# Optimization experiments

Measured on AMD Instinct MI355X. Metric: run time of the kernel, lower is better.

Reference implementation:

```python
import jax, jax.numpy as jnp
import numpy as np
import math

B, S, D, H = 2, 2048, 1024, 16
DH = D // H

def setup_inputs() -> dict:
    key = jax.random.key(0)
    ks = jax.random.split(key, 12)
    s = 1.0 / math.sqrt(D)
    return {
        "q": jax.random.normal(ks[0], (B, S, D), jnp.float32),
        "k": jax.random.normal(ks[1], (B, S, D), jnp.float32),
        "v": jax.random.normal(ks[2], (B, S, D), jnp.float32),
        "mask": jnp.tril(jnp.ones((S, S), dtype=bool)),  # causal mask
        "Wq": jax.random.normal(ks[3], (D, D), jnp.float32) * s,
        "bq": jnp.zeros((D,), jnp.float32),
        "Wk": jax.random.normal(ks[4], (D, D), jnp.float32) * s,
        "bk": jnp.zeros((D,), jnp.float32),
        "Wv": jax.random.normal(ks[5], (D, D), jnp.float32) * s,
        "bv": jnp.zeros((D,), jnp.float32),
        "Wo": jax.random.normal(ks[6], (D, D), jnp.float32) * s,
        "bo": jnp.zeros((D,), jnp.float32),
    }

def _split_heads(x):
    b, s, _ = x.shape
    return x.reshape(b, s, H, DH).transpose(0, 2, 1, 3)  # [B,H,S,DH]

def reference(q, k, v, mask, Wq, bq, Wk, bk, Wv, bv, Wo, bo):
    qh = _split_heads(q @ Wq.T + bq)
    kh = _split_heads(k @ Wk.T + bk)
    vh = _split_heads(v @ Wv.T + bv)
    scale = 1.0 / math.sqrt(DH)
    scores = jnp.einsum('bhqd,bhkd->bhqk', qh, kh) * scale  # [B,H,S,S]
    scores = jnp.where(mask[None, None, :, :], scores, -jnp.inf)
    attn = jax.nn.softmax(scores, axis=-1)
    out = jnp.einsum('bhqk,bhkd->bhqd', attn, vh)  # [B,H,S,DH]
    out = out.transpose(0, 2, 1, 3).reshape(B, S, D)  # combine heads
    return out @ Wo.T + bo
```

## Files before the change

### kernel.cpp

```cpp
#include <hip/hip_runtime.h>

typedef unsigned int u32;
typedef unsigned short u16;
typedef __attribute__((ext_vector_type(8))) short bf16x8;
typedef __attribute__((ext_vector_type(8))) u16 u16x8;
typedef __attribute__((ext_vector_type(4))) u16 u16x4;
typedef __attribute__((ext_vector_type(4))) float f32x4;
typedef __attribute__((ext_vector_type(2))) u32 u32x2;

#define AS1 __attribute__((address_space(1)))
#define AS3 __attribute__((address_space(3)))

__device__ __forceinline__ void gload_lds16(const void* g, void* l) {
  __builtin_amdgcn_global_load_lds((const AS1 u32*)g, (AS3 u32*)l, 16, 0, 0);
}

__device__ __forceinline__ u16 f2bf(float f) {
  union { float f; u32 u; } x; x.f = f;
  u32 u = x.u;
  return (u16)((u + 0x7fffu + ((u >> 16) & 1u)) >> 16);
}

__device__ __forceinline__ u32 cvt_pk_bf16(float lo, float hi) {
  u32 r;
  asm("v_cvt_pk_bf16_f32 %0, %1, %2" : "=v"(r) : "v"(lo), "v"(hi));
  return r;
}

__device__ __forceinline__ float fexp2(float x) {
  float r;
  asm("v_exp_f32 %0, %1" : "=v"(r) : "v"(x));
  return r;
}

__global__ __launch_bounds__(256) void convert_all(
    const float* __restrict__ q, const float* __restrict__ k, const float* __restrict__ v,
    const float* __restrict__ wq, const float* __restrict__ wk,
    const float* __restrict__ wv, const float* __restrict__ wo,
    u16* __restrict__ dst)
{
  int b = blockIdx.x, t = threadIdx.x;
  const float* sp; size_t lb;
  if (b < 6144) {
    sp = (b < 2048) ? q : ((b < 4096) ? k : v);
    lb = (size_t)(b & 2047) * 2048;
  } else {
    int w = (b - 6144) >> 9;
    sp = (w == 0) ? wq : ((w == 1) ? wk : ((w == 2) ? wv : wo));
    lb = (size_t)((b - 6144) & 511) * 2048;
  }
  lb += (size_t)t * 8;
  f32x4 f0 = *(const f32x4*)(sp + lb);
  f32x4 f1 = *(const f32x4*)(sp + lb + 4);
  u16x8 o;
  o[0]=f2bf(f0[0]); o[1]=f2bf(f0[1]); o[2]=f2bf(f0[2]); o[3]=f2bf(f0[3]);
  o[4]=f2bf(f1[0]); o[5]=f2bf(f1[1]); o[6]=f2bf(f1[2]); o[7]=f2bf(f1[3]);
  *(u16x8*)(dst + (size_t)b*2048 + (size_t)t*8) = o;
}

__global__ __launch_bounds__(256, 3) void gemm_qkv(
    const u16* __restrict__ Xall,
    const u16* __restrict__ Wall,
    const float* __restrict__ bq, const float* __restrict__ bk, const float* __restrict__ bv,
    u16* __restrict__ Cqk, u16* __restrict__ VT)
{
  __shared__ __align__(16) u16 lds[24576];
  const int t = threadIdx.x;
  const int wid = t >> 6, l = t & 63;
  const int c = l & 15, g = l >> 4;
  const int u = blockIdx.x;
  const int lid = (u & 7) * 96 + (u >> 3);
  const int which = lid >> 8;
  const int r5 = lid & 255;
  const int m0 = (r5 >> 3) * 128, n0 = (r5 & 7) * 128;
  const u16* A  = Xall + (size_t)which * 4194304;
  const u16* Bw = Wall + (size_t)which * 1048576;
  const int wr = wid >> 1, wc = wid & 1;

  const int srow = wid*16 + (l >> 2);
  const int sswz = ((l & 3) ^ (srow & 3) ^ ((srow >> 2) & 3)) << 3;
  const u16* Asrc0 = A  + (size_t)(m0 + srow)*1024      + sswz;
  const u16* Asrc1 = A  + (size_t)(m0 + 64 + srow)*1024 + sswz;
  const u16* Bsrc0 = Bw + (size_t)(n0 + srow)*1024      + sswz;
  const u16* Bsrc1 = Bw + (size_t)(n0 + 64 + srow)*1024 + sswz;
  const int wbase = wid * 512;

#define QKV_STAGE(j) do { \
    const int bo_ = ((j) % 3) * 8192; const int ko_ = (j) << 5; \
    gload_lds16(Asrc0 + ko_, &lds[bo_ + wbase]); \
    gload_lds16(Asrc1 + ko_, &lds[bo_ + 2048 + wbase]); \
    gload_lds16(Bsrc0 + ko_, &lds[bo_ + 4096 + wbase]); \
    gload_lds16(Bsrc1 + ko_, &lds[bo_ + 6144 + wbase]); \
  } while (0)

  const int fswz = (g ^ (c & 3) ^ ((c >> 2) & 3)) << 3;
  const int abase = (wr*64 + c)*32 + fswz;
  const int bbase = 4096 + (wc*64 + c)*32 + fswz;

  f32x4 acc[4][4] = {};

  QKV_STAGE(0);
  QKV_STAGE(1);
  asm volatile("s_waitcnt vmcnt(4)" ::: "memory");
  __builtin_amdgcn_s_barrier();
  __builtin_amdgcn_sched_barrier(0);

#pragma unroll
  for (int tstep = 0; tstep < 32; ++tstep) {
    if (tstep + 2 < 32) QKV_STAGE(tstep + 2);
    const int bo = (tstep % 3) * 8192;
    bf16x8 af[4], bf[4];
#pragma unroll
    for (int mf = 0; mf < 4; ++mf)
      af[mf] = *(const bf16x8*)&lds[bo + abase + mf*512];
#pragma unroll
    for (int nf = 0; nf < 4; ++nf)
      bf[nf] = *(const bf16x8*)&lds[bo + bbase + nf*512];
    __builtin_amdgcn_s_setprio(1);
#pragma unroll
    for (int mf = 0; mf < 4; ++mf)
#pragma unroll
      for (int nf = 0; nf < 4; ++nf)
        acc[mf][nf] = __builtin_amdgcn_mfma_f32_16x16x32_bf16(af[mf], bf[nf], acc[mf][nf], 0, 0, 0);
    __builtin_amdgcn_s_setprio(0);
    if (tstep + 2 < 32) asm volatile("s_waitcnt vmcnt(4)" ::: "memory");
    else                asm volatile("s_waitcnt vmcnt(0)" ::: "memory");
    __builtin_amdgcn_s_barrier();
    __builtin_amdgcn_sched_barrier(0);
  }
#undef QKV_STAGE

  const float* bias = (which == 0) ? bq : ((which == 1) ? bk : bv);
  if (which < 2) {
#pragma unroll
    for (int mf = 0; mf < 4; ++mf)
#pragma unroll
      for (int nf = 0; nf < 4; ++nf) {
        int row = m0 + wr*64 + mf*16 + g*4;
        int col = n0 + wc*64 + nf*16 + c;
        float bv_ = bias[col];
        int colg = which*1024 + col;
#pragma unroll
        for (int r = 0; r < 4; ++r)
          Cqk[(size_t)(row+r)*2048 + colg] = f2bf(acc[mf][nf][r] + bv_);
      }
  } else {
#pragma unroll
    for (int mf = 0; mf < 4; ++mf)
#pragma unroll
      for (int nf = 0; nf < 4; ++nf) {
        int row = m0 + wr*64 + mf*16 + g*4;
        int col = n0 + wc*64 + nf*16 + c;
        float bv_ = bias[col];
        int bb2 = row >> 11, s = row & 2047;
        int hh = col >> 6, dh = col & 63;
        u16x4 pk;
#pragma unroll
        for (int r = 0; r < 4; ++r) pk[r] = f2bf(acc[mf][nf][r] + bv_);
        *(u16x4*)&VT[((size_t)(((bb2<<4)+hh)<<6) + dh)*2048 + s] = pk;
      }
  }
}

__global__ __launch_bounds__(256) void gemm_out(
    const u16* __restrict__ A, const u16* __restrict__ Bw,
    const float* __restrict__ bias, float* __restrict__ C)
{
  __shared__ __align__(16) u16 As[128*64];
  __shared__ __align__(16) u16 Bs[64*64];
  const int t = threadIdx.x;
  const int wid = t >> 6, l = t & 63;
  const int l4 = l >> 4, l15 = l & 15;
  const int m0 = blockIdx.y * 128, n0 = blockIdx.x * 64;
  const int wr = wid >> 1, wc = wid & 1;
  const int arow = t >> 3, achk = t & 7;

  f32x4 acc[4][2] = {};

  for (int k0 = 0; k0 < 1024; k0 += 64) {
    __syncthreads();
#pragma unroll
    for (int i = 0; i < 4; ++i) {
      int row = i*32 + arow;
      gload_lds16(A + (size_t)(m0+row)*1024 + k0 + ((achk ^ (row&7)) << 3),
                  &As[i*2048 + wid*512]);
    }
#pragma unroll
    for (int i = 0; i < 2; ++i) {
      int row = i*32 + arow;
      gload_lds16(Bw + (size_t)(n0+row)*1024 + k0 + ((achk ^ (row&7)) << 3),
                  &Bs[i*2048 + wid*512]);
    }
    __syncthreads();
#pragma unroll
    for (int kh = 0; kh < 2; ++kh) {
      bf16x8 af[4], bf[2];
#pragma unroll
      for (int mf = 0; mf < 4; ++mf) {
        int row = wr*64 + mf*16 + l15;
        int ch = (kh*4 + l4) ^ (row & 7);
        af[mf] = *(const bf16x8*)&As[row*64 + ch*8];
      }
#pragma unroll
      for (int nf = 0; nf < 2; ++nf) {
        int row = wc*32 + nf*16 + l15;
        int ch = (kh*4 + l4) ^ (row & 7);
        bf[nf] = *(const bf16x8*)&Bs[row*64 + ch*8];
      }
#pragma unroll
      for (int mf = 0; mf < 4; ++mf)
#pragma unroll
        for (int nf = 0; nf < 2; ++nf)
          acc[mf][nf] = __builtin_amdgcn_mfma_f32_16x16x32_bf16(af[mf], bf[nf], acc[mf][nf], 0, 0, 0);
    }
  }
#pragma unroll
  for (int mf = 0; mf < 4; ++mf)
#pragma unroll
    for (int nf = 0; nf < 2; ++nf) {
      int row = m0 + wr*64 + mf*16 + l4*4;
      int col = n0 + wc*32 + nf*16 + l15;
      float bv = bias[col];
#pragma unroll
      for (int r = 0; r < 4; ++r)
        C[(size_t)(row+r)*1024 + col] = acc[mf][nf][r] + bv;
    }
}

__device__ __forceinline__ void stage_kv(u16* lds, const u16* Kt, const u16* Vt,
                                         int buf, int wid) {
#pragma unroll
  for (int ii = 0; ii < 2; ++ii)
    gload_lds16(Kt + (size_t)ii*32*2048, &lds[4096 + buf*4096 + ii*2048 + wid*512]);
#pragma unroll
  for (int ii = 0; ii < 2; ++ii)
    gload_lds16(Vt + (size_t)ii*32*2048, &lds[12288 + buf*4096 + ii*2048 + wid*512]);
}

__device__ __forceinline__ void attn_phase(
    u16* lds, const u16* Qg, const u16* Ka, const u16* Va,
    int q0, int kt0, int nkv, bool maskLast,
    int wid, int g, int c, int arow, int achk, int pbase, int cs,
    float& MI, float& LI, f32x4 (&o)[4])
{
  const float SC = 0.18033688f;
#pragma unroll
  for (int i = 0; i < 2; ++i) {
    int row = i*32 + arow;
    gload_lds16(Qg + (size_t)(q0+row)*2048 + ((achk ^ (row&7)) << 3),
                &lds[i*2048 + wid*512]);
  }
  const u16* Kt = Ka + (size_t)kt0 * (64*2048);
  const u16* Vt = Va + kt0 * 64;
  stage_kv(lds, Kt, Vt, 0, wid);
  asm volatile("s_waitcnt vmcnt(0)" ::: "memory");
  __builtin_amdgcn_s_barrier();
  __builtin_amdgcn_sched_barrier(0);

  bf16x8 qf[2];
#pragma unroll
  for (int kh = 0; kh < 2; ++kh) {
    int row = wid*16 + c;
    int ch = (kh*4 + g) ^ (row & 7);
    qf[kh] = *(const bf16x8*)&lds[row*64 + ch*8];
  }

  float mi = -INFINITY, li = 0.f;
#pragma unroll
  for (int df = 0; df < 4; ++df) o[df] = f32x4{0.f, 0.f, 0.f, 0.f};

  for (int i = 0; i < nkv; ++i) {
    if (i + 1 < nkv) {
      Kt += 64*2048; Vt += 64;
      stage_kv(lds, Kt, Vt, (i+1)&1, wid);
    }
    const u16* Kb = &lds[4096  + (i&1)*4096];
    const u16* Vb = &lds[12288 + (i&1)*4096];

    f32x4 sT[4] = {};
    __builtin_amdgcn_s_setprio(1);
#pragma unroll
    for (int kh = 0; kh < 2; ++kh) {
      bf16x8 kf[4];
#pragma unroll
      for (int nf = 0; nf < 4; ++nf) {
        int row = nf*16 + c;
        int ch = (kh*4 + g) ^ (c & 7);
        kf[nf] = *(const bf16x8*)&Kb[row*64 + ch*8];
      }
#pragma unroll
      for (int nf = 0; nf < 4; ++nf)
        sT[nf] = __builtin_amdgcn_mfma_f32_16x16x32_bf16(kf[nf], qf[kh], sT[nf], 0,0,0);
    }
    __builtin_amdgcn_s_setprio(0);

    if (maskLast && i == nkv - 1) {
#pragma unroll
      for (int nf = 0; nf < 4; ++nf)
#pragma unroll
        for (int r = 0; r < 4; ++r)
          if (nf*16 + g*4 + r > wid*16 + c) sT[nf][r] = -INFINITY;
    }

    float mx = fmaxf(fmaxf(sT[0][0], sT[0][1]), fmaxf(sT[0][2], sT[0][3]));
#pragma unroll
    for (int nf = 1; nf < 4; ++nf)
      mx = fmaxf(mx, fmaxf(fmaxf(sT[nf][0], sT[nf][1]), fmaxf(sT[nf][2], sT[nf][3])));
    if (!__all(mx * SC <= mi + 8.f)) {
      float mxr = fmaxf(mx, __shfl_xor(mx, 16, 64));
      mxr = fmaxf(mxr, __shfl_xor(mxr, 32, 64));
      float mn = fmaxf(mi, mxr * SC);
      float corr = fexp2(mi - mn);
      li *= corr;
#pragma unroll
      for (int df = 0; df < 4; ++df) {
        o[df][0] *= corr; o[df][1] *= corr;
        o[df][2] *= corr; o[df][3] *= corr;
      }
      mi = mn;
    }
    float sum = 0.f;
#pragma unroll
    for (int nf = 0; nf < 4; ++nf)
#pragma unroll
      for (int r = 0; r < 4; ++r) {
        float pv = fexp2(fmaf(sT[nf][r], SC, -mi));
        sT[nf][r] = pv;
        sum += pv;
      }
    li += sum;

#pragma unroll
    for (int nf = 0; nf < 4; ++nf) {
      u32x2 ww;
      ww[0] = cvt_pk_bf16(sT[nf][0], sT[nf][1]);
      ww[1] = cvt_pk_bf16(sT[nf][2], sT[nf][3]);
      int ch = (2*nf + (g >> 1)) ^ cs;
      *(u32x2*)&lds[pbase + c*64 + ch*8 + (g & 1)*4] = ww;
    }
    asm volatile("s_waitcnt lgkmcnt(0)" ::: "memory");
    __builtin_amdgcn_sched_barrier(0);

    __builtin_amdgcn_s_setprio(1);
#pragma unroll
    for (int kh = 0; kh < 2; ++kh) {
      bf16x8 pfr, vf[4];
      {
        int ch = (kh*4 + g) ^ cs;
        pfr = *(const bf16x8*)&lds[pbase + c*64 + ch*8];
      }
#pragma unroll
      for (int df = 0; df < 4; ++df) {
        int d = df*16 + c;
        int ch = (kh*4 + g) ^ (d & 7);
        vf[df] = *(const bf16x8*)&Vb[d*64 + ch*8];
      }
#pragma unroll
      for (int df = 0; df < 4; ++df)
        o[df] = __builtin_amdgcn_mfma_f32_16x16x32_bf16(vf[df], pfr, o[df], 0,0,0);
    }
    __builtin_amdgcn_s_setprio(0);

    asm volatile("s_waitcnt vmcnt(0)" ::: "memory");
    __builtin_amdgcn_s_barrier();
    __builtin_amdgcn_sched_barrier(0);
  }
  MI = mi; LI = li;
}

__device__ __forceinline__ void store_partial(
    float* __restrict__ part, int slot, int s,
    int wid, int g, int c, float mi, float li_tot, const f32x4 (&o)[4])
{
  float* po = part + (size_t)(slot*2 + s) * 4224;
  int q = wid*16 + c;
#pragma unroll
  for (int df = 0; df < 4; ++df)
    *(f32x4*)&po[q*64 + df*16 + g*4] = o[df];
  if (g == 0) { po[4096 + q] = mi; po[4160 + q] = li_tot; }
}

__global__ __launch_bounds__(256, 4) void attn_fwd(
    const u16* __restrict__ QK, const u16* __restrict__ VT,
    u16* __restrict__ AO, float* __restrict__ part)
{
  __shared__ __align__(16) u16 lds[20480];
  const int t = threadIdx.x;
  const int wid = t >> 6, l = t & 63;
  const int g = l >> 4, c = l & 15;
  const int u = blockIdx.x;
  const int lid = (u & 7) * 128 + (u >> 3);
  const int gx = lid & 31, h = (lid >> 5) & 15, b = lid >> 9;
  const int p = gx >> 1, s = gx & 1;
  const u16* Qg  = QK + (size_t)b * 2048 * 2048 + (size_t)h * 64;
  const u16* Kg  = Qg + 1024;
  const u16* VTg = VT + (size_t)(((b << 4) + h) << 6) * 2048;
  const int arow = t >> 3, achk = t & 7;
  const int pbase = wid * 1024;
  const int cs = (c & 7) ^ ((c >> 3) << 2);
  const u16* Ka = Kg  + (size_t)arow*2048 + ((achk ^ (arow & 7)) << 3);
  const u16* Va = VTg + (size_t)arow*2048 + ((achk ^ (arow & 7)) << 3);
  const int slot = ((b*16 + h)*16 + p);

  float mi, li; f32x4 o[4];

  if (s == 0) {
    attn_phase(lds, Qg, Ka, Va, p*64, 0, p+1, true,
               wid, g, c, arow, achk, pbase, cs, mi, li, o);
    {
      float lt = li + __shfl_xor(li, 16, 64);
      lt += __shfl_xor(lt, 32, 64);
      float nr = 1.f / lt;
      int row = p*64 + wid*16 + c;
      size_t rb = ((size_t)b*2048 + row)*1024 + h*64;
#pragma unroll
      for (int df = 0; df < 4; ++df) {
        u16x4 pk;
        pk[0] = f2bf(o[df][0] * nr); pk[1] = f2bf(o[df][1] * nr);
        pk[2] = f2bf(o[df][2] * nr); pk[3] = f2bf(o[df][3] * nr);
        *(u16x4*)&AO[rb + df*16 + g*4] = pk;
      }
    }
    attn_phase(lds, Qg, Ka, Va, (31-p)*64, 0, 16-p, false,
               wid, g, c, arow, achk, pbase, cs, mi, li, o);
    float lt = li + __shfl_xor(li, 16, 64);
    lt += __shfl_xor(lt, 32, 64);
    store_partial(part, slot, 0, wid, g, c, mi, lt, o);
  } else {
    attn_phase(lds, Qg, Ka, Va, (31-p)*64, 16-p, 16, true,
               wid, g, c, arow, achk, pbase, cs, mi, li, o);
    float lt = li + __shfl_xor(li, 16, 64);
    lt += __shfl_xor(lt, 32, 64);
    store_partial(part, slot, 1, wid, g, c, mi, lt, o);
  }
}

__global__ __launch_bounds__(256) void attn_merge(
    const float* __restrict__ part, u16* __restrict__ AO)
{
  int slot = blockIdx.x;
  int p = slot & 15;
  int h = (slot >> 4) & 15;
  int b = slot >> 8;
  const float* p0 = part + (size_t)slot * 8448;
  const float* p1 = p0 + 4224;
  int t = threadIdx.x;
  int r = t >> 2, c0 = (t & 3) * 16;
  float m0 = p0[4096 + r], m1 = p1[4096 + r];
  float l0 = p0[4160 + r], l1 = p1[4160 + r];
  float m = fmaxf(m0, m1);
  float e0 = exp2f(m0 - m), e1 = exp2f(m1 - m);
  float rl = 1.f / (l0*e0 + l1*e1);
  e0 *= rl; e1 *= rl;
  const f32x4* a0 = (const f32x4*)(p0 + r*64 + c0);
  const f32x4* a1 = (const f32x4*)(p1 + r*64 + c0);
  u16x8 w0, w1;
#pragma unroll
  for (int q4 = 0; q4 < 4; ++q4) {
    f32x4 x = a0[q4], y = a1[q4];
#pragma unroll
    for (int j = 0; j < 4; ++j) {
      u16 bf = f2bf(x[j]*e0 + y[j]*e1);
      if (q4 < 2) w0[q4*4+j] = bf; else w1[(q4-2)*4+j] = bf;
    }
  }
  int qrow = (31 - p)*64 + r;
  size_t ab = ((size_t)b*2048 + qrow)*1024 + h*64 + c0;
  *(u16x8*)&AO[ab]     = w0;
  *(u16x8*)&AO[ab + 8] = w1;
}

extern "C" void kernel_launch(void* const* d_in, const int* in_sizes, int n_in,
                              void* d_out, int out_size, void* d_ws, size_t ws_size,
                              hipStream_t stream)
{
  const float* q  = (const float*)d_in[0];
  const float* k  = (const float*)d_in[1];
  const float* v  = (const float*)d_in[2];
  const float* Wq = (const float*)d_in[4];
  const float* bq = (const float*)d_in[5];
  const float* Wk = (const float*)d_in[6];
  const float* bk = (const float*)d_in[7];
  const float* Wv = (const float*)d_in[8];
  const float* bv = (const float*)d_in[9];
  const float* Wo = (const float*)d_in[10];
  const float* bo = (const float*)d_in[11];
  float* out = (float*)d_out;

  u16* ws   = (u16*)d_ws;
  u16* qb   = ws;
  u16* Wqb  = ws + 12582912;
  u16* Wob  = ws + 15728640;
  u16* QKp  = ws + 16777216;
  u16* VTp  = ws + 25165824;
  u16* AO   = ws + 29360128;

  convert_all<<<8192, 256, 0, stream>>>(q, k, v, Wq, Wk, Wv, Wo, qb);

  gemm_qkv<<<768, 256, 0, stream>>>(qb, Wqb, bq, bk, bv, QKp, VTp);

  attn_fwd<<<1024, 256, 0, stream>>>(QKp, VTp, AO, (float*)d_ws);

  attn_merge<<<512, 256, 0, stream>>>((const float*)d_ws, AO);

  dim3 g1(16, 32);
  gemm_out<<<g1, 256, 0, stream>>>(AO, Wob, bo, out);
}
```

Measured before the change: 109.0 us.

## Fuse fp32-to-bf16 activation conversion into QKV GEMM and retile output GEMM

The separate pass that converted the q/k/v activations to bf16 is removed. The QKV GEMM now loads fp32 activations into registers, converts them with packed bf16 instructions and writes them into swizzled LDS, pipelined one step ahead of the MFMA loop. This avoids writing and re-reading a 12M-element bf16 intermediate, but each A tile now moves twice as many global bytes and adds register and convert work inside the GEMM loop. The output GEMM is also rewritten to reuse the triple-buffered 128x128 tile structure with an L2-friendly block remap, replacing its simpler 128x64 double-sync loop.

```diff
diff --git a/kernel.cpp b/kernel.cpp
--- a/kernel.cpp
+++ b/kernel.cpp
@@ -33,23 +33,15 @@
   return r;
 }
 
-__global__ __launch_bounds__(256) void convert_all(
-    const float* __restrict__ q, const float* __restrict__ k, const float* __restrict__ v,
+__global__ __launch_bounds__(256) void convert_w(
     const float* __restrict__ wq, const float* __restrict__ wk,
     const float* __restrict__ wv, const float* __restrict__ wo,
     u16* __restrict__ dst)
 {
   int b = blockIdx.x, t = threadIdx.x;
-  const float* sp; size_t lb;
-  if (b < 6144) {
-    sp = (b < 2048) ? q : ((b < 4096) ? k : v);
-    lb = (size_t)(b & 2047) * 2048;
-  } else {
-    int w = (b - 6144) >> 9;
-    sp = (w == 0) ? wq : ((w == 1) ? wk : ((w == 2) ? wv : wo));
-    lb = (size_t)((b - 6144) & 511) * 2048;
-  }
-  lb += (size_t)t * 8;
+  int w = b >> 9;
+  const float* sp = (w == 0) ? wq : ((w == 1) ? wk : ((w == 2) ? wv : wo));
+  size_t lb = (size_t)(b & 511) * 2048 + (size_t)t * 8;
   f32x4 f0 = *(const f32x4*)(sp + lb);
   f32x4 f1 = *(const f32x4*)(sp + lb + 4);
   u16x8 o;
@@ -59,7 +51,7 @@
 }
 
 __global__ __launch_bounds__(256, 3) void gemm_qkv(
-    const u16* __restrict__ Xall,
+    const float* __restrict__ Xq, const float* __restrict__ Xk, const float* __restrict__ Xv,
     const u16* __restrict__ Wall,
     const float* __restrict__ bq, const float* __restrict__ bk, const float* __restrict__ bv,
     u16* __restrict__ Cqk, u16* __restrict__ VT)
@@ -73,19 +65,150 @@
   const int which = lid >> 8;
   const int r5 = lid & 255;
   const int m0 = (r5 >> 3) * 128, n0 = (r5 & 7) * 128;
-  const u16* A  = Xall + (size_t)which * 4194304;
+  const float* Afp = (which == 0) ? Xq : ((which == 1) ? Xk : Xv);
   const u16* Bw = Wall + (size_t)which * 1048576;
   const int wr = wid >> 1, wc = wid & 1;
 
   const int srow = wid*16 + (l >> 2);
-  const int sswz = ((l & 3) ^ (srow & 3) ^ ((srow >> 2) & 3)) << 3;
+  const int schk = l & 3;
+  const int aswz = ((schk ^ (srow & 3) ^ ((srow >> 2) & 3)) << 3);
+  const float* Ag0 = Afp + (size_t)(m0 + srow)*1024      + schk*8;
+  const float* Ag1 = Afp + (size_t)(m0 + 64 + srow)*1024 + schk*8;
+  const int awr0 = srow*32 + aswz;
+  const int awr1 = (srow + 64)*32 + aswz;
+  const int sswz = aswz;
+  const u16* Bsrc0 = Bw + (size_t)(n0 + srow)*1024      + sswz;
+  const u16* Bsrc1 = Bw + (size_t)(n0 + 64 + srow)*1024 + sswz;
+  const int wbase = wid * 512;
+
+  f32x4 ra0, ra1, ra2, ra3;
+
+#define A_LOAD(j) do { \
+    const float* ap0_ = Ag0 + ((j) << 5); \
+    const float* ap1_ = Ag1 + ((j) << 5); \
+    ra0 = *(const f32x4*)ap0_; ra1 = *(const f32x4*)(ap0_ + 4); \
+    ra2 = *(const f32x4*)ap1_; ra3 = *(const f32x4*)(ap1_ + 4); \
+  } while (0)
+
+#define A_CVT_WRITE(j) do { \
+    const int bo_ = ((j) % 3) * 8192; \
+    u16x8 w0_, w1_; u32* q0_ = (u32*)&w0_; u32* q1_ = (u32*)&w1_; \
+    q0_[0]=cvt_pk_bf16(ra0[0],ra0[1]); q0_[1]=cvt_pk_bf16(ra0[2],ra0[3]); \
+    q0_[2]=cvt_pk_bf16(ra1[0],ra1[1]); q0_[3]=cvt_pk_bf16(ra1[2],ra1[3]); \
+    q1_[0]=cvt_pk_bf16(ra2[0],ra2[1]); q1_[1]=cvt_pk_bf16(ra2[2],ra2[3]); \
+    q1_[2]=cvt_pk_bf16(ra3[0],ra3[1]); q1_[3]=cvt_pk_bf16(ra3[2],ra3[3]); \
+    *(u16x8*)&lds[bo_ + awr0] = w0_; \
+    *(u16x8*)&lds[bo_ + awr1] = w1_; \
+  } while (0)
+
+#define B_STAGE(j) do { \
+    const int bo_ = ((j) % 3) * 8192; const int ko_ = (j) << 5; \
+    gload_lds16(Bsrc0 + ko_, &lds[bo_ + 4096 + wbase]); \
+    gload_lds16(Bsrc1 + ko_, &lds[bo_ + 6144 + wbase]); \
+  } while (0)
+
+  const int fswz = (g ^ (c & 3) ^ ((c >> 2) & 3)) << 3;
+  const int abase = (wr*64 + c)*32 + fswz;
+  const int bbase = 4096 + (wc*64 + c)*32 + fswz;
+
+  f32x4 acc[4][4] = {};
+
+  A_LOAD(0);
+  B_STAGE(0);
+  B_STAGE(1);
+  asm volatile("s_waitcnt vmcnt(2)" ::: "memory");
+  A_CVT_WRITE(0);
+  A_LOAD(1);
+  asm volatile("s_waitcnt lgkmcnt(0)" ::: "memory");
+  __builtin_amdgcn_s_barrier();
+  __builtin_amdgcn_sched_barrier(0);
+
+#pragma unroll
+  for (int tstep = 0; tstep < 32; ++tstep) {
+    if (tstep + 2 < 32) B_STAGE(tstep + 2);
+    const int bo = (tstep % 3) * 8192;
+    bf16x8 af[4], bf[4];
+#pragma unroll
+    for (int mf = 0; mf < 4; ++mf)
+      af[mf] = *(const bf16x8*)&lds[bo + abase + mf*512];
+#pragma unroll
+    for (int nf = 0; nf < 4; ++nf)
+      bf[nf] = *(const bf16x8*)&lds[bo + bbase + nf*512];
+    __builtin_amdgcn_s_setprio(1);
+#pragma unroll
+    for (int mf = 0; mf < 4; ++mf)
+#pragma unroll
+      for (int nf = 0; nf < 4; ++nf)
+        acc[mf][nf] = __builtin_amdgcn_mfma_f32_16x16x32_bf16(af[mf], bf[nf], acc[mf][nf], 0, 0, 0);
+    __builtin_amdgcn_s_setprio(0);
+    if (tstep + 1 < 32) {
+      if (tstep + 2 < 32) asm volatile("s_waitcnt vmcnt(2)" ::: "memory");
+      else                asm volatile("s_waitcnt vmcnt(0)" ::: "memory");
+      A_CVT_WRITE(tstep + 1);
+      if (tstep + 2 < 32) A_LOAD(tstep + 2);
+    }
+    asm volatile("s_waitcnt lgkmcnt(0)" ::: "memory");
+    __builtin_amdgcn_s_barrier();
+    __builtin_amdgcn_sched_barrier(0);
+  }
+#undef A_LOAD
+#undef A_CVT_WRITE
+#undef B_STAGE
+
+  const float* bias = (which == 0) ? bq : ((which == 1) ? bk : bv);
+  if (which < 2) {
+#pragma unroll
+    for (int mf = 0; mf < 4; ++mf)
+#pragma unroll
+      for (int nf = 0; nf < 4; ++nf) {
+        int row = m0 + wr*64 + mf*16 + g*4;
+        int col = n0 + wc*64 + nf*16 + c;
+        float bv_ = bias[col];
+        int colg = which*1024 + col;
+#pragma unroll
+        for (int r = 0; r < 4; ++r)
+          Cqk[(size_t)(row+r)*2048 + colg] = f2bf(acc[mf][nf][r] + bv_);
+      }
+  } else {
+#pragma unroll
+    for (int mf = 0; mf < 4; ++mf)
+#pragma unroll
+      for (int nf = 0; nf < 4; ++nf) {
+        int row = m0 + wr*64 + mf*16 + g*4;
+        int col = n0 + wc*64 + nf*16 + c;
+        float bv_ = bias[col];
+        int bb2 = row >> 11, s = row & 2047;
+        int hh = col >> 6, dh = col & 63;
+        u16x4 pk;
+#pragma unroll
+        for (int r = 0; r < 4; ++r) pk[r] = f2bf(acc[mf][nf][r] + bv_);
+        *(u16x4*)&VT[((size_t)(((bb2<<4)+hh)<<6) + dh)*2048 + s] = pk;
+      }
+  }
+}
+
+__global__ __launch_bounds__(256, 3) void gemm_out(
+    const u16* __restrict__ A, const u16* __restrict__ Bw,
+    const float* __restrict__ bias, float* __restrict__ C)
+{
+  __shared__ __align__(16) u16 lds[24576];
+  const int t = threadIdx.x;
+  const int wid = t >> 6, l = t & 63;
+  const int c = l & 15, g = l >> 4;
+  const int u = blockIdx.x;
+  const int lid = (u & 7) * 32 + (u >> 3);
+  const int m0 = (lid >> 3) * 128, n0 = (lid & 7) * 128;
+  const int wr = wid >> 1, wc = wid & 1;
+
+  const int srow = wid*16 + (l >> 2);
+  const int sswz = (((l & 3) ^ (srow & 3) ^ ((srow >> 2) & 3)) << 3);
   const u16* Asrc0 = A  + (size_t)(m0 + srow)*1024      + sswz;
   const u16* Asrc1 = A  + (size_t)(m0 + 64 + srow)*1024 + sswz;
   const u16* Bsrc0 = Bw + (size_t)(n0 + srow)*1024      + sswz;
   const u16* Bsrc1 = Bw + (size_t)(n0 + 64 + srow)*1024 + sswz;
   const int wbase = wid * 512;
 
-#define QKV_STAGE(j) do { \
+#define O_STAGE(j) do { \
     const int bo_ = ((j) % 3) * 8192; const int ko_ = (j) << 5; \
     gload_lds16(Asrc0 + ko_, &lds[bo_ + wbase]); \
     gload_lds16(Asrc1 + ko_, &lds[bo_ + 2048 + wbase]); \
@@ -99,15 +222,15 @@
 
   f32x4 acc[4][4] = {};
 
-  QKV_STAGE(0);
-  QKV_STAGE(1);
+  O_STAGE(0);
+  O_STAGE(1);
   asm volatile("s_waitcnt vmcnt(4)" ::: "memory");
   __builtin_amdgcn_s_barrier();
   __builtin_amdgcn_sched_barrier(0);
 
 #pragma unroll
   for (int tstep = 0; tstep < 32; ++tstep) {
-    if (tstep + 2 < 32) QKV_STAGE(tstep + 2);
+    if (tstep + 2 < 32) O_STAGE(tstep + 2);
     const int bo = (tstep % 3) * 8192;
     bf16x8 af[4], bf[4];
 #pragma unroll
@@ -128,102 +251,18 @@
     __builtin_amdgcn_s_barrier();
     __builtin_amdgcn_sched_barrier(0);
   }
-#undef QKV_STAGE
-
-  const float* bias = (which == 0) ? bq : ((which == 1) ? bk : bv);
-  if (which < 2) {
-#pragma unroll
-    for (int mf = 0; mf < 4; ++mf)
-#pragma unroll
-      for (int nf = 0; nf < 4; ++nf) {
-        int row = m0 + wr*64 + mf*16 + g*4;
-        int col = n0 + wc*64 + nf*16 + c;
-        float bv_ = bias[col];
-        int colg = which*1024 + col;
-#pragma unroll
-        for (int r = 0; r < 4; ++r)
-          Cqk[(size_t)(row+r)*2048 + colg] = f2bf(acc[mf][nf][r] + bv_);
-      }
-  } else {
-#pragma unroll
-    for (int mf = 0; mf < 4; ++mf)
-#pragma unroll
-      for (int nf = 0; nf < 4; ++nf) {
-        int row = m0 + wr*64 + mf*16 + g*4;
-        int col = n0 + wc*64 + nf*16 + c;
-        float bv_ = bias[col];
-        int bb2 = row >> 11, s = row & 2047;
-        int hh = col >> 6, dh = col & 63;
-        u16x4 pk;
-#pragma unroll
-        for (int r = 0; r < 4; ++r) pk[r] = f2bf(acc[mf][nf][r] + bv_);
-        *(u16x4*)&VT[((size_t)(((bb2<<4)+hh)<<6) + dh)*2048 + s] = pk;
-      }
-  }
-}
-
-__global__ __launch_bounds__(256) void gemm_out(
-    const u16* __restrict__ A, const u16* __restrict__ Bw,
-    const float* __restrict__ bias, float* __restrict__ C)
-{
-  __shared__ __align__(16) u16 As[128*64];
-  __shared__ __align__(16) u16 Bs[64*64];
-  const int t = threadIdx.x;
-  const int wid = t >> 6, l = t & 63;
-  const int l4 = l >> 4, l15 = l & 15;
-  const int m0 = blockIdx.y * 128, n0 = blockIdx.x * 64;
-  const int wr = wid >> 1, wc = wid & 1;
-  const int arow = t >> 3, achk = t & 7;
-
-  f32x4 acc[4][2] = {};
-
-  for (int k0 = 0; k0 < 1024; k0 += 64) {
-    __syncthreads();
-#pragma unroll
-    for (int i = 0; i < 4; ++i) {
-      int row = i*32 + arow;
-      gload_lds16(A + (size_t)(m0+row)*1024 + k0 + ((achk ^ (row&7)) << 3),
-                  &As[i*2048 + wid*512]);
-    }
-#pragma unroll
-    for (int i = 0; i < 2; ++i) {
-      int row = i*32 + arow;
-      gload_lds16(Bw + (size_t)(n0+row)*1024 + k0 + ((achk ^ (row&7)) << 3),
-                  &Bs[i*2048 + wid*512]);
-    }
-    __syncthreads();
-#pragma unroll
-    for (int kh = 0; kh < 2; ++kh) {
-      bf16x8 af[4], bf[2];
-#pragma unroll
-      for (int mf = 0; mf < 4; ++mf) {
-        int row = wr*64 + mf*16 + l15;
-        int ch = (kh*4 + l4) ^ (row & 7);
-        af[mf] = *(const bf16x8*)&As[row*64 + ch*8];
-      }
-#pragma unroll
-      for (int nf = 0; nf < 2; ++nf) {
-        int row = wc*32 + nf*16 + l15;
-        int ch = (kh*4 + l4) ^ (row & 7);
-        bf[nf] = *(const bf16x8*)&Bs[row*64 + ch*8];
-      }
-#pragma unroll
-      for (int mf = 0; mf < 4; ++mf)
-#pragma unroll
-        for (int nf = 0; nf < 2; ++nf)
-          acc[mf][nf] = __builtin_amdgcn_mfma_f32_16x16x32_bf16(af[mf], bf[nf], acc[mf][nf], 0, 0, 0);
-    }
-  }
+#undef O_STAGE
+
 #pragma unroll
   for (int mf = 0; mf < 4; ++mf)
 #pragma unroll
-    for (int nf = 0; nf < 2; ++nf) {
-      int row = m0 + wr*64 + mf*16 + l4*4;
-      int col = n0 + wc*32 + nf*16 + l15;
-      float bv = bias[col];
+    for (int nf = 0; nf < 4; ++nf) {
+      int row = m0 + wr*64 + mf*16 + g*4;
+      int col = n0 + wc*64 + nf*16 + c;
+      float bv_ = bias[col];
 #pragma unroll
       for (int r = 0; r < 4; ++r)
-        C[(size_t)(row+r)*1024 + col] = acc[mf][nf][r] + bv;
+        C[(size_t)(row+r)*1024 + col] = acc[mf][nf][r] + bv_;
     }
 }
 
@@ -488,21 +527,19 @@
   float* out = (float*)d_out;
 
   u16* ws   = (u16*)d_ws;
-  u16* qb   = ws;
   u16* Wqb  = ws + 12582912;
   u16* Wob  = ws + 15728640;
   u16* QKp  = ws + 16777216;
   u16* VTp  = ws + 25165824;
   u16* AO   = ws + 29360128;
 
-  convert_all<<<8192, 256, 0, stream>>>(q, k, v, Wq, Wk, Wv, Wo, qb);
-
-  gemm_qkv<<<768, 256, 0, stream>>>(qb, Wqb, bq, bk, bv, QKp, VTp);
+  convert_w<<<2048, 256, 0, stream>>>(Wq, Wk, Wv, Wo, Wqb);
+
+  gemm_qkv<<<768, 256, 0, stream>>>(q, k, v, Wqb, bq, bk, bv, QKp, VTp);
 
   attn_fwd<<<1024, 256, 0, stream>>>(QKp, VTp, AO, (float*)d_ws);
 
   attn_merge<<<512, 256, 0, stream>>>((const float*)d_ws, AO);
 
-  dim3 g1(16, 32);
-  gemm_out<<<g1, 256, 0, stream>>>(AO, Wob, bo, out);
-}
+  gemm_out<<<256, 256, 0, stream>>>(AO, Wob, bo, out);
+}
```

Measured after the change: 101.8 us. -6.6%, faster.
